# Kernel tuning notes

Hardware: AMD Instinct MI355X
Metric: run time of the kernel (lower is better)

## Reference

```python
import jax, jax.numpy as jnp
import numpy as np

SCALE = 0.1
TEMP = 1.0
LN_EPS = 1e-6
NORM_EPS = 1e-12  # torch F.normalize eps

def setup_inputs() -> dict:
    key = jax.random.key(0)
    k1, = jax.random.split(key, 1)
    x = jax.random.normal(k1, (8192, 512), dtype=jnp.float32)
    gamma = jnp.ones((512,), dtype=jnp.float32)
    beta = jnp.zeros((512,), dtype=jnp.float32)
    return {"x": x, "gamma": gamma, "beta": beta}

def reference(x, gamma, beta):
    # L2-normalize rows (torch F.normalize semantics: x / max(||x||, eps))
    norm = jnp.maximum(jnp.linalg.norm(x, axis=1, keepdims=True), NORM_EPS)
    xn = x / norm                                   # [N, d]
    sim = (xn @ xn.T) / TEMP                        # [N, N]
    # dual_norm: row softmax + column softmax
    sim = jax.nn.softmax(sim, axis=1) + jax.nn.softmax(sim, axis=0)
    x_neg = sim @ x                                 # [N, d]
    y = x - SCALE * x_neg
    # LayerNorm over last dim, eps=1e-6
    mean = jnp.mean(y, axis=-1, keepdims=True)
    var = jnp.mean(jnp.square(y - mean), axis=-1, keepdims=True)
    out = (y - mean) * jax.lax.rsqrt(var + LN_EPS) * gamma + beta
    return out
```

## Files before the change

kernel.cpp:

```cpp
#include <hip/hip_runtime.h>
#include <math.h>

#define NN 8192
#define DD 512

constexpr float SCALE_C = 0.1f;
constexpr float LN_EPS_C = 1e-6f;
constexpr float NORM_EPS_C = 1e-12f;
constexpr float CBIG = 32768.0f;
constexpr float INV_CBIG = 1.0f / 32768.0f;

typedef __attribute__((ext_vector_type(8))) short bf16x8;
typedef __attribute__((ext_vector_type(4))) float f32x4;

#define MFMA16(a, b, c) __builtin_amdgcn_mfma_f32_16x16x32_bf16((a), (b), (c), 0, 0, 0)
#define MFMA8(a, b, c)                                                        \
  __builtin_amdgcn_mfma_f32_16x16x32_fp8_fp8((long)(a), (long)(b), (c), 0, 0, 0)

#define GLL16(g, l)                                                        \
  __builtin_amdgcn_global_load_lds(                                        \
      (const __attribute__((address_space(1))) unsigned int*)(g),          \
      (__attribute__((address_space(3))) unsigned int*)(l), 16, 0, 0)

#define WAITV4() asm volatile("s_waitcnt vmcnt(4)" ::: "memory")
#define WAITV0() asm volatile("s_waitcnt vmcnt(0)" ::: "memory")
#define WAITLGKM0() asm volatile("s_waitcnt lgkmcnt(0)" ::: "memory")
#define FENCE() asm volatile("" ::: "memory")
#define BAR() __builtin_amdgcn_s_barrier()

__device__ inline unsigned short f2bf(float f) {
  unsigned int u = __builtin_bit_cast(unsigned int, f);
  unsigned int r = (u + 0x7FFFu + ((u >> 16) & 1u)) >> 16;
  return (unsigned short)r;
}

__device__ inline unsigned int f2fp8n(float f) {
  unsigned int a = __builtin_bit_cast(unsigned int, f);
  unsigned int r = a + 0x7FFFFu + ((a >> 20) & 1u);
  return (r >> 20) - 960u;
}

__device__ inline unsigned int f2fp8(float f) {
  unsigned int u = __builtin_bit_cast(unsigned int, f);
  unsigned int s = (u >> 24) & 0x80u;
  unsigned int a = u & 0x7fffffffu;
  if (a >= 0x3C800000u) {
    unsigned int r = a + 0x7FFFFu + ((a >> 20) & 1u);
    return s | ((r >> 20) - 960u);
  }
  float af = __builtin_bit_cast(float, a);
  return s | (unsigned int)(int)rintf(af * 512.0f);
}

__device__ inline float fp82f(unsigned int b) {
  return __builtin_bit_cast(float, (b + 960u) << 20);
}

__global__ __launch_bounds__(128) void k_prep(const float* __restrict__ x,
                                              unsigned short* __restrict__ xnb) {
  const int row = blockIdx.x;
  const int t = threadIdx.x;
  float4 v = ((const float4*)(x + (size_t)row * DD))[t];
  float ss = v.x * v.x + v.y * v.y + v.z * v.z + v.w * v.w;
#pragma unroll
  for (int off = 32; off; off >>= 1) ss += __shfl_down(ss, off);
  __shared__ float red[2];
  if ((t & 63) == 0) red[t >> 6] = ss;
  __syncthreads();
  float rn = 1.0f / fmaxf(sqrtf(red[0] + red[1]), NORM_EPS_C);
  ushort4 o;
  o.x = f2bf(v.x * rn);
  o.y = f2bf(v.y * rn);
  o.z = f2bf(v.z * rn);
  o.w = f2bf(v.w * rn);
  ((ushort4*)(xnb + (size_t)row * DD))[t] = o;
}

__global__ __launch_bounds__(256) void k_tr(const float* __restrict__ x,
                                            unsigned char* __restrict__ xT8) {
  __shared__ unsigned char T8[64][68];
  const int j0 = blockIdx.x * 64;
  const int d0 = blockIdx.y * 64;
  const int t = threadIdx.x;
#pragma unroll
  for (int q = 0; q < 4; ++q) {
    int f = t + q * 256;
    int r = f >> 4, c4 = f & 15;
    float4 v = *(const float4*)&x[(size_t)(j0 + r) * DD + d0 + c4 * 4];
    unsigned int w = f2fp8(v.x) | (f2fp8(v.y) << 8) | (f2fp8(v.z) << 16) |
                     (f2fp8(v.w) << 24);
    *(unsigned int*)&T8[r][c4 * 4] = w;
  }
  __syncthreads();
  {
    const int d = t >> 2, j16 = t & 3;
    unsigned int w[4];
#pragma unroll
    for (int p = 0; p < 4; ++p) {
      w[p] = (unsigned int)T8[j16 * 16 + p * 4 + 0][d] |
             ((unsigned int)T8[j16 * 16 + p * 4 + 1][d] << 8) |
             ((unsigned int)T8[j16 * 16 + p * 4 + 2][d] << 16) |
             ((unsigned int)T8[j16 * 16 + p * 4 + 3][d] << 24);
    }
    uint4 o = make_uint4(w[0], w[1], w[2], w[3]);
    *(uint4*)&xT8[(size_t)(d0 + d) * NN + j0 + j16 * 16] = o;
  }
}

__global__ __launch_bounds__(256, 4) void k_rowsumE(const unsigned short* __restrict__ xnb,
                                                    float* __restrict__ lpart,
                                                    unsigned char* __restrict__ E8) {
  __shared__ __align__(16) unsigned char POOL[32768];
  __shared__ float red[4][64];
  __shared__ float red2[4][64];

  int b = blockIdx.x, bi = 0;
  while (b >= 64 - bi) { b -= 64 - bi; ++bi; }
  const int bj = bi + b;
  const int i0 = bi * 128, j0 = bj * 128;
  const int diag = (bi == bj);

  const int t = threadIdx.x;
  const int w = t >> 6, l = t & 63;
  const int lr = l & 15, lg = l >> 4;
  const int wr = w >> 1, wc = w & 1;
  const int r0 = w * 16 + (l >> 2);
  const int clog = (l & 3) ^ ((r0 >> 1) & 3);
  const unsigned short* gA = xnb + (size_t)(i0 + r0) * DD + clog * 8;
  const unsigned short* gB = xnb + (size_t)(j0 + r0) * DD + clog * 8;

#define RS_STAGE(s, koff)                                                        \
  do {                                                                           \
    GLL16(gA + (koff), (unsigned short*)(POOL + (s) * 16384) + w * 512);         \
    GLL16(gA + (size_t)64 * DD + (koff),                                         \
          (unsigned short*)(POOL + (s) * 16384 + 4096) + w * 512);               \
    GLL16(gB + (koff), (unsigned short*)(POOL + (s) * 16384 + 8192) + w * 512);  \
    GLL16(gB + (size_t)64 * DD + (koff),                                         \
          (unsigned short*)(POOL + (s) * 16384 + 12288) + w * 512);              \
  } while (0)

  RS_STAGE(0, 0);
  RS_STAGE(1, 32);

  f32x4 acc[4][4] = {};
  for (int ks = 0; ks < 16; ++ks) {
    if (ks + 1 < 16) { WAITV4(); } else { WAITV0(); }
    BAR(); FENCE();
    const char* AS = (const char*)(POOL + (ks & 1) * 16384);
    const char* BS = AS + 8192;
    bf16x8 af[4], bv[4];
#pragma unroll
    for (int fm = 0; fm < 4; ++fm) {
      const int row = wr * 64 + fm * 16 + lr;
      af[fm] = *(const bf16x8*)(AS + row * 64 + ((lg ^ ((row >> 1) & 3)) << 4));
    }
#pragma unroll
    for (int fn = 0; fn < 4; ++fn) {
      const int row = wc * 64 + fn * 16 + lr;
      bv[fn] = *(const bf16x8*)(BS + row * 64 + ((lg ^ ((row >> 1) & 3)) << 4));
    }
    WAITLGKM0();
    BAR(); FENCE();
    if (ks + 2 < 16) RS_STAGE(ks & 1, (size_t)(ks + 2) * 32);
#pragma unroll
    for (int fm = 0; fm < 4; ++fm)
#pragma unroll
      for (int fn = 0; fn < 4; ++fn)
        acc[fm][fn] = MFMA16(af[fm], bv[fn], acc[fm][fn]);
  }

  unsigned int ebw[4][4];
  float rsum[4][4] = {};
  float csum[4] = {};
#pragma unroll
  for (int fm = 0; fm < 4; ++fm)
#pragma unroll
    for (int fn = 0; fn < 4; ++fn) {
      unsigned int pw = 0;
#pragma unroll
      for (int rr = 0; rr < 4; ++rr) {
        float e = __expf(acc[fm][fn][rr]);
        rsum[fm][rr] += e;
        csum[fn] += e;
        pw |= f2fp8n(e) << (8 * rr);
      }
      ebw[fm][fn] = pw;
    }

#pragma unroll
  for (int fm = 0; fm < 4; ++fm)
#pragma unroll
    for (int rr = 0; rr < 4; ++rr) {
      float s = rsum[fm][rr];
#pragma unroll
      for (int off = 1; off < 16; off <<= 1) s += __shfl_xor(s, off);
      if (lr == 0) red[w][fm * 16 + lg * 4 + rr] = s;
    }
  if (!diag) {
#pragma unroll
    for (int fn = 0; fn < 4; ++fn) {
      float cs = csum[fn];
      cs += __shfl_xor(cs, 16);
      cs += __shfl_xor(cs, 32);
      if (lg == 0) red2[w][fn * 16 + lr] = cs;
    }
  }

  unsigned char(*Et)[144] = (unsigned char(*)[144])POOL;
#pragma unroll
  for (int fm = 0; fm < 4; ++fm)
#pragma unroll
    for (int fn = 0; fn < 4; ++fn) {
#pragma unroll
      for (int rr = 0; rr < 4; ++rr)
        Et[wr * 64 + fm * 16 + lg * 4 + rr][wc * 64 + fn * 16 + lr] =
            (unsigned char)((ebw[fm][fn] >> (8 * rr)) & 0xffu);
    }
  __syncthreads();
  {
    unsigned char* dst = E8 + ((size_t)(bi * 64 + bj) << 14);
#pragma unroll
    for (int q = 0; q < 4; ++q) {
      const int f = t + q * 256;
      *(uint4*)(dst + f * 16) = *(const uint4*)&Et[f >> 3][(f & 7) * 16];
    }
  }
  if (t < 128) {
    const int wrx = t >> 6, idx = t & 63;
    lpart[(size_t)bj * NN + i0 + t] = red[2 * wrx][idx] + red[2 * wrx + 1][idx];
  } else if (!diag) {
    const int c = t - 128;
    const int wcx = c >> 6, idx = c & 63;
    lpart[(size_t)bi * NN + j0 + c] = red2[wcx][idx] + red2[2 + wcx][idx];
  }
}

__global__ __launch_bounds__(256) void k_recip(const float* __restrict__ lpart,
                                               float* __restrict__ rl) {
  const int i = blockIdx.x * 256 + threadIdx.x;
  float s = 0.f;
  for (int c = 0; c < 64; ++c) s += lpart[(size_t)c * NN + i];
  rl[i] = CBIG / s;
}

__global__ __launch_bounds__(256) void k_scale2(unsigned char* __restrict__ P,
                                                const float* __restrict__ rl) {
  __shared__ unsigned int T32[128][35];
  int b = blockIdx.x, ti = 0;
  while (b >= 64 - ti) { b -= 64 - ti; ++ti; }
  const int tj = ti + b;
  const int i0 = ti * 128, j0 = tj * 128;
  const int t = threadIdx.x;
  unsigned char* tileC = P + ((size_t)(ti * 64 + tj) << 14);

#pragma unroll
  for (int q = 0; q < 4; ++q) {
    const int f = t + q * 256;
    const int r = f >> 3;
    const int c0 = (f & 7) * 16;
    uint4 v = *(const uint4*)(tileC + f * 16);
    const float rli = rl[i0 + r];
    float rlj[16];
#pragma unroll
    for (int p = 0; p < 4; ++p) {
      float4 r4 = *(const float4*)(rl + j0 + c0 + p * 4);
      rlj[p * 4 + 0] = r4.x; rlj[p * 4 + 1] = r4.y;
      rlj[p * 4 + 2] = r4.z; rlj[p * 4 + 3] = r4.w;
    }
    unsigned int wsrc[4] = {v.x, v.y, v.z, v.w};
    unsigned int wdst[4];
#pragma unroll
    for (int p = 0; p < 4; ++p) {
      unsigned int in = wsrc[p], out = 0;
#pragma unroll
      for (int k = 0; k < 4; ++k) {
        float e = fp82f((in >> (8 * k)) & 0xffu);
        out |= f2fp8n(e * (rli + rlj[p * 4 + k])) << (8 * k);
      }
      wdst[p] = out;
      T32[r][(c0 >> 2) + p] = out;
    }
    *(uint4*)(tileC + f * 16) = make_uint4(wdst[0], wdst[1], wdst[2], wdst[3]);
  }
  if (ti == tj) return;
  __syncthreads();

  unsigned char* tileT = P + ((size_t)(tj * 64 + ti) << 14);
  {
    const int rg = t >> 3;
    const int cc = t & 7;
    const int c2 = cc * 16;
    unsigned int o[4][4];
#pragma unroll
    for (int k4 = 0; k4 < 4; ++k4) {
      unsigned int a0 = T32[c2 + k4 * 4 + 0][rg];
      unsigned int a1 = T32[c2 + k4 * 4 + 1][rg];
      unsigned int a2 = T32[c2 + k4 * 4 + 2][rg];
      unsigned int a3 = T32[c2 + k4 * 4 + 3][rg];
      unsigned int b0 = (a0 & 0x00FF00FFu) | ((a1 << 8) & 0xFF00FF00u);
      unsigned int b1 = ((a0 >> 8) & 0x00FF00FFu) | (a1 & 0xFF00FF00u);
      unsigned int b2 = (a2 & 0x00FF00FFu) | ((a3 << 8) & 0xFF00FF00u);
      unsigned int b3 = ((a2 >> 8) & 0x00FF00FFu) | (a3 & 0xFF00FF00u);
      o[0][k4] = (b0 & 0x0000FFFFu) | (b2 << 16);
      o[1][k4] = (b1 & 0x0000FFFFu) | (b3 << 16);
      o[2][k4] = (b0 >> 16) | (b2 & 0xFFFF0000u);
      o[3][k4] = (b1 >> 16) | (b3 & 0xFFFF0000u);
    }
#pragma unroll
    for (int i = 0; i < 4; ++i)
      *(uint4*)(tileT + (size_t)(rg * 4 + i) * 128 + c2) =
          make_uint4(o[i][0], o[i][1], o[i][2], o[i][3]);
  }
}

__global__ __launch_bounds__(256, 4) void k_pv3(const unsigned char* __restrict__ P8,
                                                const unsigned char* __restrict__ xT8,
                                                unsigned short* __restrict__ parts) {
  __shared__ __align__(16) unsigned char As[2][8192];
  __shared__ __align__(16) unsigned char Bs[2][8192];
  const int i0 = blockIdx.x * 128;
  const int n0 = blockIdx.y * 128;
  const int z = blockIdx.z;
  const int t = threadIdx.x;
  const int w = t >> 6, l = t & 63;
  const int lr = l & 15, lg = l >> 4;
  const int wr = w >> 1, wc = w & 1;
  const int r0 = w * 16 + (l >> 2);
  const int clog = (l & 3) ^ ((r0 >> 1) & 3);
  const unsigned char* Abase = P8 + ((size_t)((i0 >> 7) * 64 + z * 16) << 14) +
                               r0 * 128 + clog * 16;
  const unsigned char* gB = xT8 + (size_t)(n0 + r0) * NN + z * 2048 + clog * 16;

#define PV_STAGE(s, koff)                                                      \
  do {                                                                         \
    const unsigned char* a_ = Abase + (((koff) >> 7) << 14) + ((koff) & 127);  \
    GLL16(a_, &As[s][w * 1024]);                                               \
    GLL16(a_ + 8192, &As[s][4096 + w * 1024]);                                 \
    GLL16(gB + (koff), &Bs[s][w * 1024]);                                      \
    GLL16(gB + (size_t)64 * NN + (koff), &Bs[s][4096 + w * 1024]);             \
  } while (0)

  PV_STAGE(0, 0);
  PV_STAGE(1, 64);

  f32x4 acc[4][4] = {};
  for (int ks = 0; ks < 32; ++ks) {
    if (ks + 1 < 32) { WAITV4(); } else { WAITV0(); }
    BAR(); FENCE();
    const char* AS = (const char*)&As[ks & 1][0];
    const char* BS = (const char*)&Bs[ks & 1][0];
    unsigned long long af[4][2], bv[4][2];
#pragma unroll
    for (int fm = 0; fm < 4; ++fm) {
      const int row = wr * 64 + fm * 16 + lr;
      const int swz = (row >> 1) & 3;
#pragma unroll
      for (int kk = 0; kk < 2; ++kk) {
        int off = row * 64 + (((kk * 2 + (lg >> 1)) ^ swz) << 4) + ((lg & 1) << 3);
        af[fm][kk] = *(const unsigned long long*)(AS + off);
      }
    }
#pragma unroll
    for (int fn = 0; fn < 4; ++fn) {
      const int row = wc * 64 + fn * 16 + lr;
      const int swz = (row >> 1) & 3;
#pragma unroll
      for (int kk = 0; kk < 2; ++kk) {
        int off = row * 64 + (((kk * 2 + (lg >> 1)) ^ swz) << 4) + ((lg & 1) << 3);
        bv[fn][kk] = *(const unsigned long long*)(BS + off);
      }
    }
    WAITLGKM0();
    BAR(); FENCE();
    if (ks + 2 < 32) PV_STAGE(ks & 1, (ks + 2) * 64);
#pragma unroll
    for (int kk = 0; kk < 2; ++kk)
#pragma unroll
      for (int fm = 0; fm < 4; ++fm)
#pragma unroll
        for (int fn = 0; fn < 4; ++fn)
          acc[fm][fn] = MFMA8(af[fm][kk], bv[fn][kk], acc[fm][fn]);
  }
  unsigned short* dst = parts + (size_t)z * NN * DD;
#pragma unroll
  for (int fm = 0; fm < 4; ++fm)
#pragma unroll
    for (int fn = 0; fn < 4; ++fn)
#pragma unroll
      for (int rr = 0; rr < 4; ++rr)
        dst[(size_t)(i0 + wr * 64 + fm * 16 + lg * 4 + rr) * DD + n0 + wc * 64 +
            fn * 16 + lr] = f2bf(acc[fm][fn][rr] * INV_CBIG);
}

__global__ __launch_bounds__(128) void k_ln(const float* __restrict__ x,
                                            float* __restrict__ out,
                                            const unsigned short* __restrict__ parts,
                                            const float* __restrict__ gamma,
                                            const float* __restrict__ beta) {
  const int row = blockIdx.x;
  const int t = threadIdx.x;
  float4 p = make_float4(0.f, 0.f, 0.f, 0.f);
#pragma unroll
  for (int s = 0; s < 4; ++s) {
    ushort4 q = ((const ushort4*)(parts + (size_t)s * NN * DD + (size_t)row * DD))[t];
    p.x += __builtin_bit_cast(float, (unsigned int)q.x << 16);
    p.y += __builtin_bit_cast(float, (unsigned int)q.y << 16);
    p.z += __builtin_bit_cast(float, (unsigned int)q.z << 16);
    p.w += __builtin_bit_cast(float, (unsigned int)q.w << 16);
  }
  float4 xv = ((const float4*)(x + (size_t)row * DD))[t];
  float4 y;
  y.x = xv.x - SCALE_C * p.x;
  y.y = xv.y - SCALE_C * p.y;
  y.z = xv.z - SCALE_C * p.z;
  y.w = xv.w - SCALE_C * p.w;
  float sum = y.x + y.y + y.z + y.w;
#pragma unroll
  for (int off = 32; off; off >>= 1) sum += __shfl_down(sum, off);
  __shared__ float ra[2], rb[2];
  if ((t & 63) == 0) ra[t >> 6] = sum;
  __syncthreads();
  float mean = (ra[0] + ra[1]) * (1.0f / DD);
  float d0 = y.x - mean, d1 = y.y - mean, d2 = y.z - mean, d3 = y.w - mean;
  float vs = d0 * d0 + d1 * d1 + d2 * d2 + d3 * d3;
#pragma unroll
  for (int off = 32; off; off >>= 1) vs += __shfl_down(vs, off);
  if ((t & 63) == 0) rb[t >> 6] = vs;
  __syncthreads();
  float rstd = rsqrtf((rb[0] + rb[1]) * (1.0f / DD) + LN_EPS_C);
  float4 g4 = ((const float4*)gamma)[t];
  float4 b4 = ((const float4*)beta)[t];
  float4 o;
  o.x = d0 * rstd * g4.x + b4.x;
  o.y = d1 * rstd * g4.y + b4.y;
  o.z = d2 * rstd * g4.z + b4.z;
  o.w = d3 * rstd * g4.w + b4.w;
  ((float4*)(out + (size_t)row * DD))[t] = o;
}

extern "C" void kernel_launch(void* const* d_in, const int* in_sizes, int n_in,
                              void* d_out, int out_size, void* d_ws, size_t ws_size,
                              hipStream_t stream) {
  const float* x = (const float*)d_in[0];
  const float* gamma = (const float*)d_in[1];
  const float* beta = (const float*)d_in[2];
  float* out = (float*)d_out;

  unsigned short* xnb = (unsigned short*)d_ws;
  unsigned char* xT8 = (unsigned char*)(xnb + (size_t)NN * DD);
  float* lpart = (float*)(xT8 + (size_t)NN * DD);
  float* rl = lpart + (size_t)64 * NN;
  unsigned short* parts = (unsigned short*)(rl + NN);
  unsigned char* E8 = (unsigned char*)(parts + (size_t)4 * NN * DD);

  k_prep<<<NN, 128, 0, stream>>>(x, xnb);
  k_tr<<<dim3(NN / 64, DD / 64), 256, 0, stream>>>(x, xT8);
  k_rowsumE<<<2080, 256, 0, stream>>>(xnb, lpart, E8);
  k_recip<<<NN / 256, 256, 0, stream>>>(lpart, rl);
  k_scale2<<<2080, 256, 0, stream>>>(E8, rl);
  k_pv3<<<dim3(64, 4, 4), 256, 0, stream>>>(E8, xT8, parts);
  k_ln<<<NN, 128, 0, stream>>>(x, out, parts, gamma, beta);
}
```

Baseline: 153.8 us.

## Triple-buffer A tiles in LDS and load B fragments directly to registers

Restructures the k_rowsumE GEMM main loop. The A tile now uses a 3-stage LDS ring with one barrier per k-step. B fragments are loaded straight from global memory into double-buffered registers, which removes the B share of LDS traffic and the second barrier. It also fully unrolls the loop, raises wave priority around the MFMA block, and remaps block indices to spread tiles across XCDs. In exchange it uses more registers and its correctness depends on hand-tuned vmcnt wait counts.

```diff
diff --git a/kernel.cpp b/kernel.cpp
--- a/kernel.cpp
+++ b/kernel.cpp
@@ -22,6 +22,7 @@
       (const __attribute__((address_space(1))) unsigned int*)(g),          \
       (__attribute__((address_space(3))) unsigned int*)(l), 16, 0, 0)
 
+#define WAITV6() asm volatile("s_waitcnt vmcnt(6)" ::: "memory")
 #define WAITV4() asm volatile("s_waitcnt vmcnt(4)" ::: "memory")
 #define WAITV0() asm volatile("s_waitcnt vmcnt(0)" ::: "memory")
 #define WAITLGKM0() asm volatile("s_waitcnt lgkmcnt(0)" ::: "memory")
@@ -110,11 +111,12 @@
 __global__ __launch_bounds__(256, 4) void k_rowsumE(const unsigned short* __restrict__ xnb,
                                                     float* __restrict__ lpart,
                                                     unsigned char* __restrict__ E8) {
-  __shared__ __align__(16) unsigned char POOL[32768];
+  __shared__ __align__(16) unsigned char POOL[24576];
   __shared__ float red[4][64];
   __shared__ float red2[4][64];
 
-  int b = blockIdx.x, bi = 0;
+  int b = (blockIdx.x & 7) * 260 + (blockIdx.x >> 3);
+  int bi = 0;
   while (b >= 64 - bi) { b -= 64 - bi; ++bi; }
   const int bj = bi + b;
   const int i0 = bi * 128, j0 = bj * 128;
@@ -127,47 +129,46 @@
   const int r0 = w * 16 + (l >> 2);
   const int clog = (l & 3) ^ ((r0 >> 1) & 3);
   const unsigned short* gA = xnb + (size_t)(i0 + r0) * DD + clog * 8;
-  const unsigned short* gB = xnb + (size_t)(j0 + r0) * DD + clog * 8;
-
-#define RS_STAGE(s, koff)                                                        \
-  do {                                                                           \
-    GLL16(gA + (koff), (unsigned short*)(POOL + (s) * 16384) + w * 512);         \
-    GLL16(gA + (size_t)64 * DD + (koff),                                         \
-          (unsigned short*)(POOL + (s) * 16384 + 4096) + w * 512);               \
-    GLL16(gB + (koff), (unsigned short*)(POOL + (s) * 16384 + 8192) + w * 512);  \
-    GLL16(gB + (size_t)64 * DD + (koff),                                         \
-          (unsigned short*)(POOL + (s) * 16384 + 12288) + w * 512);              \
+  const unsigned short* gBr = xnb + (size_t)(j0 + wc * 64 + lr) * DD + lg * 8;
+
+#define RS_STAGE(s, kt)                                                        \
+  do {                                                                         \
+    GLL16(gA + (kt) * 32, (unsigned short*)(POOL + (s) * 8192) + w * 512);     \
+    GLL16(gA + (size_t)64 * DD + (kt) * 32,                                    \
+          (unsigned short*)(POOL + (s) * 8192 + 4096) + w * 512);              \
   } while (0)
 
+#define B_LOAD(dst, kt)                                                        \
+  do {                                                                         \
+    _Pragma("unroll") for (int fn = 0; fn < 4; ++fn)(dst)[fn] =                \
+        *(const bf16x8*)(gBr + (size_t)fn * 16 * DD + (kt) * 32);              \
+  } while (0)
+
   RS_STAGE(0, 0);
-  RS_STAGE(1, 32);
+  bf16x8 bv[2][4];
+  B_LOAD(bv[0], 0);
+  RS_STAGE(1, 1);
 
   f32x4 acc[4][4] = {};
+#pragma unroll
   for (int ks = 0; ks < 16; ++ks) {
-    if (ks + 1 < 16) { WAITV4(); } else { WAITV0(); }
+    if (ks == 15) { WAITV4(); } else { WAITV6(); }
     BAR(); FENCE();
-    const char* AS = (const char*)(POOL + (ks & 1) * 16384);
-    const char* BS = AS + 8192;
-    bf16x8 af[4], bv[4];
+    if (ks + 1 < 16) B_LOAD(bv[(ks + 1) & 1], ks + 1);
+    if (ks + 2 < 16) RS_STAGE((ks + 2) % 3, ks + 2);
+    const char* AS = (const char*)(POOL + (ks % 3) * 8192);
+    __builtin_amdgcn_s_setprio(1);
 #pragma unroll
     for (int fm = 0; fm < 4; ++fm) {
       const int row = wr * 64 + fm * 16 + lr;
-      af[fm] = *(const bf16x8*)(AS + row * 64 + ((lg ^ ((row >> 1) & 3)) << 4));
-    }
-#pragma unroll
-    for (int fn = 0; fn < 4; ++fn) {
-      const int row = wc * 64 + fn * 16 + lr;
-      bv[fn] = *(const bf16x8*)(BS + row * 64 + ((lg ^ ((row >> 1) & 3)) << 4));
-    }
-    WAITLGKM0();
-    BAR(); FENCE();
-    if (ks + 2 < 16) RS_STAGE(ks & 1, (size_t)(ks + 2) * 32);
-#pragma unroll
-    for (int fm = 0; fm < 4; ++fm)
+      bf16x8 af = *(const bf16x8*)(AS + row * 64 + ((lg ^ ((row >> 1) & 3)) << 4));
 #pragma unroll
       for (int fn = 0; fn < 4; ++fn)
-        acc[fm][fn] = MFMA16(af[fm], bv[fn], acc[fm][fn]);
-  }
+        acc[fm][fn] = MFMA16(af, bv[ks & 1][fn], acc[fm][fn]);
+    }
+    __builtin_amdgcn_s_setprio(0);
+  }
+  BAR(); FENCE();
 
   unsigned int ebw[4][4];
   float rsum[4][4] = {};
```

Result: slower. 181.6 us (+18.1%).

## Remap blocks for XCD L2 locality and fold reciprocal into scale kernel

Applied to the files above, without the earlier changes.

Permutes block indices in the rowsum and PV kernels so blocks sharing input tiles land on the same XCD and reuse its L2. Removes the separate reciprocal kernel by having each scale block sum the 64 partial row sums for its 256 rows into shared memory. This saves a launch and a round trip through global memory. In exchange, every scale block repeats the column reductions, which adds redundant L2 reads.

```diff
diff --git a/kernel.cpp b/kernel.cpp
--- a/kernel.cpp
+++ b/kernel.cpp
@@ -114,7 +114,8 @@
   __shared__ float red[4][64];
   __shared__ float red2[4][64];
 
-  int b = blockIdx.x, bi = 0;
+  int b = (blockIdx.x & 7) * 260 + (blockIdx.x >> 3);
+  int bi = 0;
   while (b >= 64 - bi) { b -= 64 - bi; ++bi; }
   const int bj = bi + b;
   const int i0 = bi * 128, j0 = bj * 128;
@@ -235,23 +236,25 @@
   }
 }
 
-__global__ __launch_bounds__(256) void k_recip(const float* __restrict__ lpart,
-                                               float* __restrict__ rl) {
-  const int i = blockIdx.x * 256 + threadIdx.x;
-  float s = 0.f;
-  for (int c = 0; c < 64; ++c) s += lpart[(size_t)c * NN + i];
-  rl[i] = CBIG / s;
-}
-
 __global__ __launch_bounds__(256) void k_scale2(unsigned char* __restrict__ P,
-                                                const float* __restrict__ rl) {
+                                                const float* __restrict__ lpart) {
   __shared__ unsigned int T32[128][35];
+  __shared__ float rls[256];
   int b = blockIdx.x, ti = 0;
   while (b >= 64 - ti) { b -= 64 - ti; ++ti; }
   const int tj = ti + b;
   const int i0 = ti * 128, j0 = tj * 128;
   const int t = threadIdx.x;
   unsigned char* tileC = P + ((size_t)(ti * 64 + tj) << 14);
+
+  {
+    const int row = (t < 128) ? (i0 + t) : (j0 + t - 128);
+    float s = 0.f;
+#pragma unroll 8
+    for (int c = 0; c < 64; ++c) s += lpart[(size_t)c * NN + row];
+    rls[t] = CBIG / s;
+  }
+  __syncthreads();
 
 #pragma unroll
   for (int q = 0; q < 4; ++q) {
@@ -259,14 +262,7 @@
     const int r = f >> 3;
     const int c0 = (f & 7) * 16;
     uint4 v = *(const uint4*)(tileC + f * 16);
-    const float rli = rl[i0 + r];
-    float rlj[16];
-#pragma unroll
-    for (int p = 0; p < 4; ++p) {
-      float4 r4 = *(const float4*)(rl + j0 + c0 + p * 4);
-      rlj[p * 4 + 0] = r4.x; rlj[p * 4 + 1] = r4.y;
-      rlj[p * 4 + 2] = r4.z; rlj[p * 4 + 3] = r4.w;
-    }
+    const float rli = rls[r];
     unsigned int wsrc[4] = {v.x, v.y, v.z, v.w};
     unsigned int wdst[4];
 #pragma unroll
@@ -275,7 +271,7 @@
 #pragma unroll
       for (int k = 0; k < 4; ++k) {
         float e = fp82f((in >> (8 * k)) & 0xffu);
-        out |= f2fp8n(e * (rli + rlj[p * 4 + k])) << (8 * k);
+        out |= f2fp8n(e * (rli + rls[128 + c0 + p * 4 + k])) << (8 * k);
       }
       wdst[p] = out;
       T32[r][(c0 >> 2) + p] = out;
@@ -318,9 +314,15 @@
                                                 unsigned short* __restrict__ parts) {
   __shared__ __align__(16) unsigned char As[2][8192];
   __shared__ __align__(16) unsigned char Bs[2][8192];
-  const int i0 = blockIdx.x * 128;
-  const int n0 = blockIdx.y * 128;
-  const int z = blockIdx.z;
+  const int L = blockIdx.x;
+  const int xcd = L & 7;
+  const int rr_ = L >> 3;
+  const int s_ = rr_ & 3;
+  const int q_ = rr_ >> 2;
+  const int a_ = xcd + 8 * q_;
+  const int i0 = (a_ & 63) * 128;
+  const int z = a_ >> 6;
+  const int n0 = s_ * 128;
   const int t = threadIdx.x;
   const int w = t >> 6, l = t & 63;
   const int lr = l & 15, lg = l >> 4;
@@ -333,9 +335,9 @@
 
 #define PV_STAGE(s, koff)                                                      \
   do {                                                                         \
-    const unsigned char* a_ = Abase + (((koff) >> 7) << 14) + ((koff) & 127);  \
-    GLL16(a_, &As[s][w * 1024]);                                               \
-    GLL16(a_ + 8192, &As[s][4096 + w * 1024]);                                 \
+    const unsigned char* a_p = Abase + (((koff) >> 7) << 14) + ((koff) & 127); \
+    GLL16(a_p, &As[s][w * 1024]);                                              \
+    GLL16(a_p + 8192, &As[s][4096 + w * 1024]);                                \
     GLL16(gB + (koff), &Bs[s][w * 1024]);                                      \
     GLL16(gB + (size_t)64 * NN + (koff), &Bs[s][4096 + w * 1024]);             \
   } while (0)
@@ -449,15 +451,14 @@
   unsigned short* xnb = (unsigned short*)d_ws;
   unsigned char* xT8 = (unsigned char*)(xnb + (size_t)NN * DD);
   float* lpart = (float*)(xT8 + (size_t)NN * DD);
-  float* rl = lpart + (size_t)64 * NN;
-  unsigned short* parts = (unsigned short*)(rl + NN);
+  float* rl_unused = lpart + (size_t)64 * NN;
+  unsigned short* parts = (unsigned short*)(rl_unused + NN);
   unsigned char* E8 = (unsigned char*)(parts + (size_t)4 * NN * DD);
 
   k_prep<<<NN, 128, 0, stream>>>(x, xnb);
   k_tr<<<dim3(NN / 64, DD / 64), 256, 0, stream>>>(x, xT8);
   k_rowsumE<<<2080, 256, 0, stream>>>(xnb, lpart, E8);
-  k_recip<<<NN / 256, 256, 0, stream>>>(lpart, rl);
-  k_scale2<<<2080, 256, 0, stream>>>(E8, rl);
-  k_pv3<<<dim3(64, 4, 4), 256, 0, stream>>>(E8, xT8, parts);
+  k_scale2<<<2080, 256, 0, stream>>>(E8, lpart);
+  k_pv3<<<1024, 256, 0, stream>>>(E8, xT8, parts);
   k_ln<<<NN, 128, 0, stream>>>(x, out, parts, gamma, beta);
 }
```

Result: no change. 155.1 us (+0.9%).

## Fuse normalize and fp8 transpose prep kernels; store E tiles transposed with word writes

Applied to the files above, without the earlier changes.

Merges the row-normalize bf16 kernel and the fp8 transpose kernel into one pass, so x is read once and one launch is dropped. Each block handles 16 rows and writes 16-byte column chunks of xT8. The rowsum kernel now writes each E tile transposed into the mirrored tile slot using 32-bit LDS stores instead of byte stores, and the scale kernel swaps its tile indexing and rl roles to match. The fused kernel launches only 512 blocks, and its xT8 stores are 16-byte chunks strided by NN, which may coalesce less well.

```diff
diff --git a/kernel.cpp b/kernel.cpp
--- a/kernel.cpp
+++ b/kernel.cpp
@@ -56,54 +56,49 @@
   return __builtin_bit_cast(float, (b + 960u) << 20);
 }
 
-__global__ __launch_bounds__(128) void k_prep(const float* __restrict__ x,
-                                              unsigned short* __restrict__ xnb) {
-  const int row = blockIdx.x;
+__global__ __launch_bounds__(256) void k_prep2(const float* __restrict__ x,
+                                               unsigned short* __restrict__ xnb,
+                                               unsigned char* __restrict__ xT8) {
+  __shared__ unsigned int T8w[16][130];
+  const int j0 = blockIdx.x * 16;
   const int t = threadIdx.x;
-  float4 v = ((const float4*)(x + (size_t)row * DD))[t];
-  float ss = v.x * v.x + v.y * v.y + v.z * v.z + v.w * v.w;
-#pragma unroll
-  for (int off = 32; off; off >>= 1) ss += __shfl_down(ss, off);
-  __shared__ float red[2];
-  if ((t & 63) == 0) red[t >> 6] = ss;
+  const int tr = t >> 4, tc = t & 15;
+  const int row = j0 + tr;
+  const float* xr = x + (size_t)row * DD;
+  float4 v[8];
+  float ss = 0.f;
+#pragma unroll
+  for (int k = 0; k < 8; ++k) {
+    v[k] = *(const float4*)(xr + tc * 4 + k * 64);
+    ss += v[k].x * v[k].x + v[k].y * v[k].y + v[k].z * v[k].z + v[k].w * v[k].w;
+  }
+#pragma unroll
+  for (int off = 1; off < 16; off <<= 1) ss += __shfl_xor(ss, off);
+  const float rn = 1.0f / fmaxf(sqrtf(ss), NORM_EPS_C);
+#pragma unroll
+  for (int k = 0; k < 8; ++k) {
+    ushort4 o;
+    o.x = f2bf(v[k].x * rn);
+    o.y = f2bf(v[k].y * rn);
+    o.z = f2bf(v[k].z * rn);
+    o.w = f2bf(v[k].w * rn);
+    *(ushort4*)(xnb + (size_t)row * DD + tc * 4 + k * 64) = o;
+    T8w[tr][tc + k * 16] = f2fp8(v[k].x) | (f2fp8(v[k].y) << 8) |
+                           (f2fp8(v[k].z) << 16) | (f2fp8(v[k].w) << 24);
+  }
   __syncthreads();
-  float rn = 1.0f / fmaxf(sqrtf(red[0] + red[1]), NORM_EPS_C);
-  ushort4 o;
-  o.x = f2bf(v.x * rn);
-  o.y = f2bf(v.y * rn);
-  o.z = f2bf(v.z * rn);
-  o.w = f2bf(v.w * rn);
-  ((ushort4*)(xnb + (size_t)row * DD))[t] = o;
-}
-
-__global__ __launch_bounds__(256) void k_tr(const float* __restrict__ x,
-                                            unsigned char* __restrict__ xT8) {
-  __shared__ unsigned char T8[64][68];
-  const int j0 = blockIdx.x * 64;
-  const int d0 = blockIdx.y * 64;
-  const int t = threadIdx.x;
-#pragma unroll
-  for (int q = 0; q < 4; ++q) {
-    int f = t + q * 256;
-    int r = f >> 4, c4 = f & 15;
-    float4 v = *(const float4*)&x[(size_t)(j0 + r) * DD + d0 + c4 * 4];
-    unsigned int w = f2fp8(v.x) | (f2fp8(v.y) << 8) | (f2fp8(v.z) << 16) |
-                     (f2fp8(v.w) << 24);
-    *(unsigned int*)&T8[r][c4 * 4] = w;
-  }
-  __syncthreads();
-  {
-    const int d = t >> 2, j16 = t & 3;
-    unsigned int w[4];
-#pragma unroll
-    for (int p = 0; p < 4; ++p) {
-      w[p] = (unsigned int)T8[j16 * 16 + p * 4 + 0][d] |
-             ((unsigned int)T8[j16 * 16 + p * 4 + 1][d] << 8) |
-             ((unsigned int)T8[j16 * 16 + p * 4 + 2][d] << 16) |
-             ((unsigned int)T8[j16 * 16 + p * 4 + 3][d] << 24);
-    }
-    uint4 o = make_uint4(w[0], w[1], w[2], w[3]);
-    *(uint4*)&xT8[(size_t)(d0 + d) * NN + j0 + j16 * 16] = o;
+#pragma unroll
+  for (int q = 0; q < 2; ++q) {
+    const int d = t + q * 256;
+    const unsigned char* col = (const unsigned char*)&T8w[0][0] + d;
+    unsigned int wds[4];
+#pragma unroll
+    for (int p = 0; p < 4; ++p)
+      wds[p] = (unsigned int)col[(p * 4 + 0) * 520] |
+               ((unsigned int)col[(p * 4 + 1) * 520] << 8) |
+               ((unsigned int)col[(p * 4 + 2) * 520] << 16) |
+               ((unsigned int)col[(p * 4 + 3) * 520] << 24);
+    *(uint4*)&xT8[(size_t)d * NN + j0] = make_uint4(wds[0], wds[1], wds[2], wds[3]);
   }
 }
 
@@ -206,23 +201,20 @@
     }
   }
 
-  unsigned char(*Et)[144] = (unsigned char(*)[144])POOL;
+  unsigned char(*Et2)[144] = (unsigned char(*)[144])POOL;
 #pragma unroll
   for (int fm = 0; fm < 4; ++fm)
 #pragma unroll
-    for (int fn = 0; fn < 4; ++fn) {
-#pragma unroll
-      for (int rr = 0; rr < 4; ++rr)
-        Et[wr * 64 + fm * 16 + lg * 4 + rr][wc * 64 + fn * 16 + lr] =
-            (unsigned char)((ebw[fm][fn] >> (8 * rr)) & 0xffu);
-    }
+    for (int fn = 0; fn < 4; ++fn)
+      *(unsigned int*)&Et2[wc * 64 + fn * 16 + lr][wr * 64 + fm * 16 + lg * 4] =
+          ebw[fm][fn];
   __syncthreads();
   {
-    unsigned char* dst = E8 + ((size_t)(bi * 64 + bj) << 14);
+    unsigned char* dst2 = E8 + ((size_t)(bj * 64 + bi) << 14);
 #pragma unroll
     for (int q = 0; q < 4; ++q) {
       const int f = t + q * 256;
-      *(uint4*)(dst + f * 16) = *(const uint4*)&Et[f >> 3][(f & 7) * 16];
+      *(uint4*)(dst2 + f * 16) = *(const uint4*)&Et2[f >> 3][(f & 7) * 16];
     }
   }
   if (t < 128) {
@@ -251,7 +243,7 @@
   const int tj = ti + b;
   const int i0 = ti * 128, j0 = tj * 128;
   const int t = threadIdx.x;
-  unsigned char* tileC = P + ((size_t)(ti * 64 + tj) << 14);
+  unsigned char* tileC = P + ((size_t)(tj * 64 + ti) << 14);
 
 #pragma unroll
   for (int q = 0; q < 4; ++q) {
@@ -259,13 +251,13 @@
     const int r = f >> 3;
     const int c0 = (f & 7) * 16;
     uint4 v = *(const uint4*)(tileC + f * 16);
-    const float rli = rl[i0 + r];
-    float rlj[16];
+    const float rlr = rl[j0 + r];
+    float rlc[16];
 #pragma unroll
     for (int p = 0; p < 4; ++p) {
-      float4 r4 = *(const float4*)(rl + j0 + c0 + p * 4);
-      rlj[p * 4 + 0] = r4.x; rlj[p * 4 + 1] = r4.y;
-      rlj[p * 4 + 2] = r4.z; rlj[p * 4 + 3] = r4.w;
+      float4 r4 = *(const float4*)(rl + i0 + c0 + p * 4);
+      rlc[p * 4 + 0] = r4.x; rlc[p * 4 + 1] = r4.y;
+      rlc[p * 4 + 2] = r4.z; rlc[p * 4 + 3] = r4.w;
     }
     unsigned int wsrc[4] = {v.x, v.y, v.z, v.w};
     unsigned int wdst[4];
@@ -275,7 +267,7 @@
 #pragma unroll
       for (int k = 0; k < 4; ++k) {
         float e = fp82f((in >> (8 * k)) & 0xffu);
-        out |= f2fp8n(e * (rli + rlj[p * 4 + k])) << (8 * k);
+        out |= f2fp8n(e * (rlr + rlc[p * 4 + k])) << (8 * k);
       }
       wdst[p] = out;
       T32[r][(c0 >> 2) + p] = out;
@@ -285,7 +277,7 @@
   if (ti == tj) return;
   __syncthreads();
 
-  unsigned char* tileT = P + ((size_t)(tj * 64 + ti) << 14);
+  unsigned char* tileT = P + ((size_t)(ti * 64 + tj) << 14);
   {
     const int rg = t >> 3;
     const int cc = t & 7;
@@ -453,8 +445,7 @@
   unsigned short* parts = (unsigned short*)(rl + NN);
   unsigned char* E8 = (unsigned char*)(parts + (size_t)4 * NN * DD);
 
-  k_prep<<<NN, 128, 0, stream>>>(x, xnb);
-  k_tr<<<dim3(NN / 64, DD / 64), 256, 0, stream>>>(x, xT8);
+  k_prep2<<<NN / 16, 256, 0, stream>>>(x, xnb, xT8);
   k_rowsumE<<<2080, 256, 0, stream>>>(xnb, lpart, E8);
   k_recip<<<NN / 256, 256, 0, stream>>>(lpart, rl);
   k_scale2<<<2080, 256, 0, stream>>>(E8, rl);
```

New measurement: 150.8 us. 2.0% less time.
